# Optimization experiments

Hardware: AMD Instinct MI355X
Metric: run time of the kernel (lower is better)

## Reference

```python
import jax, jax.numpy as jnp
import numpy as np

D_MODEL = 1024
NUM_HEADS = 16
HEAD_DIM = D_MODEL // NUM_HEADS
B, T = 2, 2048


def setup_inputs() -> dict:
    key = jax.random.key(0)
    k1, k2, k3, k4, k5 = jax.random.split(key, 5)
    s = 1.0 / np.sqrt(D_MODEL)
    x = jax.random.normal(k1, (B, T, D_MODEL), dtype=jnp.float32)
    mask = jnp.ones((B, T), dtype=jnp.int32)
    W_qkv = jax.random.uniform(k2, (D_MODEL, 3 * D_MODEL), jnp.float32, -s, s)
    b_qkv = jax.random.uniform(k3, (3 * D_MODEL,), jnp.float32, -s, s)
    W_out = jax.random.uniform(k4, (D_MODEL, D_MODEL), jnp.float32, -s, s)
    b_out = jax.random.uniform(k5, (D_MODEL,), jnp.float32, -s, s)
    return {"x": x, "mask": mask, "W_qkv": W_qkv, "b_qkv": b_qkv,
            "W_out": W_out, "b_out": b_out}


def reference(x, mask, W_qkv, b_qkv, W_out, b_out):
    Bv, Tv, Dv = x.shape
    scale = HEAD_DIM ** -0.5
    qkv = x @ W_qkv + b_qkv                       # [B,T,3D]
    qkv = qkv.reshape(Bv, Tv, 3, NUM_HEADS, HEAD_DIM)
    qkv = jnp.transpose(qkv, (2, 0, 3, 1, 4))     # [3,B,H,T,hd]
    q, k, v = qkv[0], qkv[1], qkv[2]
    scores = jnp.einsum('bhqd,bhkd->bhqk', q, k) * scale  # [B,H,T,T]
    m = mask[:, None, None, :]                    # [B,1,1,T]
    scores = jnp.where(m == 0, -jnp.inf, scores)
    attn = jax.nn.softmax(scores, axis=-1)
    out = jnp.einsum('bhqk,bhkd->bhqd', attn, v)  # [B,H,T,hd]
    out = jnp.transpose(out, (0, 2, 1, 3)).reshape(Bv, Tv, Dv)
    return out @ W_out + b_out
```

## Files before the change

### kernel.cpp

```cpp
#include <hip/hip_runtime.h>

typedef __bf16 bf16;
typedef __bf16 bf16x8 __attribute__((ext_vector_type(8)));
typedef __bf16 bf16x4 __attribute__((ext_vector_type(4)));
typedef float  f32x4  __attribute__((ext_vector_type(4)));
typedef float  f32x16 __attribute__((ext_vector_type(16)));
typedef unsigned int u32x4 __attribute__((ext_vector_type(4)));

#define MFMA16(a, b, c) __builtin_amdgcn_mfma_f32_16x16x32_bf16((a), (b), (c), 0, 0, 0)
#define MFMA32(a, b, c) __builtin_amdgcn_mfma_f32_32x32x16_bf16((a), (b), (c), 0, 0, 0)

__device__ __forceinline__ float fexp2(float x) {
  return __builtin_amdgcn_exp2f(x);
}

__device__ __forceinline__ unsigned cvt_pk_bf16(float lo, float hi) {
  unsigned r;
  asm("v_cvt_pk_bf16_f32 %0, %1, %2" : "=v"(r) : "v"(lo), "v"(hi));
  return r;
}

__device__ __forceinline__ void gload_lds16(const bf16* g, bf16* l) {
  __builtin_amdgcn_global_load_lds(
      (const __attribute__((address_space(1))) void*)g,
      (__attribute__((address_space(3))) void*)l, 16, 0, 0);
}


__global__ __launch_bounds__(256) void cast_bf16_kernel(
    const float* __restrict__ in, bf16* __restrict__ out, int n4) {
  int i = blockIdx.x * 256 + threadIdx.x;
  if (i < n4) {
    float4 v = reinterpret_cast<const float4*>(in)[i];
    bf16x4 o;
    o[0] = (bf16)v.x; o[1] = (bf16)v.y; o[2] = (bf16)v.z; o[3] = (bf16)v.w;
    reinterpret_cast<bf16x4*>(out)[i] = o;
  }
}

__global__ __launch_bounds__(256) void transpose_cast_kernel(
    const float* __restrict__ W, bf16* __restrict__ Wt, int K, int N) {
  __shared__ bf16 tile[64 * 66];
  const int k0 = blockIdx.y * 64, n0 = blockIdx.x * 64;
  const int c = threadIdx.x & 63, rb = threadIdx.x >> 6;
#pragma unroll
  for (int p = 0; p < 16; ++p) {
    int r = p * 4 + rb;
    tile[c * 66 + r] = (bf16)W[(long)(k0 + r) * N + n0 + c];
  }
  __syncthreads();
#pragma unroll
  for (int p = 0; p < 16; ++p) {
    int r = p * 4 + rb;
    Wt[(long)(n0 + r) * K + k0 + c] = tile[r * 66 + c];
  }
}

template <int EPI>
__global__ __launch_bounds__(256, 2) void gemm_bt(
    const bf16* __restrict__ A, const bf16* __restrict__ Bt,
    const float* __restrict__ bias, bf16* __restrict__ oQ,
    bf16* __restrict__ oK, bf16* __restrict__ oVT, float* __restrict__ oC,
    int K) {
  __shared__ bf16 As[128 * 64];
  __shared__ bf16 Bs[128 * 64];
  const int tid = threadIdx.x, lane = tid & 63, wid = tid >> 6;
  const int wr = wid >> 1, wc = wid & 1;
  const int brow = blockIdx.x * 128, bcol = blockIdx.y * 128;
  const int srow = lane >> 3, scol8 = (lane & 7) * 8;
  const int c15 = lane & 15, g = lane >> 4;

  f32x4 acc[4][4];
#pragma unroll
  for (int m = 0; m < 4; ++m)
#pragma unroll
    for (int n = 0; n < 4; ++n) acc[m][n] = f32x4{0.f, 0.f, 0.f, 0.f};

  const bf16* Ab = A + (long)brow * K + scol8;
  const bf16* Bb = Bt + (long)bcol * K + scol8;

  for (int k0 = 0; k0 < K; k0 += 64) {
#pragma unroll
    for (int i = 0; i < 4; ++i) {
      int c = wid * 4 + i;
      int row = c * 8 + srow;
      gload_lds16(Ab + (long)row * K + k0, &As[c * 512]);
    }
#pragma unroll
    for (int i = 0; i < 4; ++i) {
      int c = wid * 4 + i;
      int row = c * 8 + srow;
      gload_lds16(Bb + (long)row * K + k0, &Bs[c * 512]);
    }
    __syncthreads();
#pragma unroll
    for (int kk = 0; kk < 64; kk += 32) {
      bf16x8 a[4], b[4];
#pragma unroll
      for (int m = 0; m < 4; ++m)
        a[m] = *(const bf16x8*)&As[(wr * 64 + m * 16 + c15) * 64 + kk + g * 8];
#pragma unroll
      for (int n = 0; n < 4; ++n)
        b[n] = *(const bf16x8*)&Bs[(wc * 64 + n * 16 + c15) * 64 + kk + g * 8];
#pragma unroll
      for (int m = 0; m < 4; ++m)
#pragma unroll
        for (int n = 0; n < 4; ++n)
          acc[m][n] = MFMA16(a[m], b[n], acc[m][n]);
    }
    __syncthreads();
  }

#pragma unroll
  for (int n = 0; n < 4; ++n) {
    const int col = bcol + wc * 64 + n * 16 + c15;
    const float bv = bias[col];
    if (EPI == 0) {
      const int which = col >> 10, wi = col & 1023, h = wi >> 6, d = wi & 63;
      const float sc = (which == 0) ? 0.18033688011112042f : 1.0f;
#pragma unroll
      for (int m = 0; m < 4; ++m) {
        const int row0 = brow + wr * 64 + m * 16 + g * 4;
        const int bb = row0 >> 11, t0 = row0 & 2047;
        const long hb = bb * 16 + h;
        if (which == 2) {
          bf16x4 pv;
#pragma unroll
          for (int r = 0; r < 4; ++r) pv[r] = (bf16)(acc[m][n][r] + bv);
          *(bf16x4*)&oVT[(hb * 64 + d) * 2048 + t0] = pv;
        } else {
          bf16* dst = ((which == 0) ? oQ : oK) + (hb * 2048 + t0) * 64 + d;
#pragma unroll
          for (int r = 0; r < 4; ++r)
            dst[(long)r * 64] = (bf16)((acc[m][n][r] + bv) * sc);
        }
      }
    } else {
#pragma unroll
      for (int m = 0; m < 4; ++m) {
        const long row = brow + wr * 64 + m * 16 + g * 4;
#pragma unroll
        for (int r = 0; r < 4; ++r) oC[(row + r) * 1024 + col] = acc[m][n][r] + bv;
      }
    }
  }
}

__global__ __launch_bounds__(256, 4) void attn_kernel(
    const bf16* __restrict__ Q, const bf16* __restrict__ K,
    const bf16* __restrict__ VT, const int* __restrict__ mask,
    float* __restrict__ O_part, float* __restrict__ ml_part) {
  __shared__ bf16 Kl[2][4096];
  __shared__ bf16 Vl[2][4096];
  __shared__ float sws[4][32];
  const int tid = threadIdx.x, lane = tid & 63, w = tid >> 6;
  const int col = lane & 31, hi = lane >> 5, c7 = col & 7;
  const int bid = blockIdx.x;
  const int swz = (bid & 7) * 128 + (bid >> 3);
  const int bh = swz >> 5, rem = swz & 31;
  const int s = rem & 1, qb = rem >> 1;
  const int b = bh >> 4, h = bh & 15;
  const int q0 = qb * 128 + w * 32;
  const int koff0 = s * 1024;

  const bf16* Kbase = K + (long)bh * 2048 * 64;
  const bf16* Vbase = VT + (long)bh * 64 * 2048;
  const int* mb = mask + b * 2048;

  const int srow = lane >> 3;
  const int xoff = ((lane & 7) ^ srow) << 3;

  auto stage = [&](int buf, int t) {
    const int koff = koff0 + t * 64;
#pragma unroll
    for (int i = 0; i < 2; ++i) {
      const int c = w * 2 + i;
      gload_lds16(Kbase + (long)(koff + c * 8 + srow) * 64 + xoff,
                  &Kl[buf][c * 512]);
      gload_lds16(Vbase + (long)(c * 8 + srow) * 2048 + koff + xoff,
                  &Vl[buf][c * 512]);
    }
  };

  const bf16* Qp = Q + ((long)bh * 2048 + q0 + col) * 64 + hi * 8;
  bf16x8 bq[4];
#pragma unroll
  for (int dc = 0; dc < 4; ++dc) bq[dc] = *(const bf16x8*)(Qp + dc * 16);

  f32x16 o0, o1;
#pragma unroll
  for (int r = 0; r < 16; ++r) { o0[r] = 0.f; o1[r] = 0.f; }
  float mrun = -1e30f, lrun = 0.f;

  stage(0, 0);
  for (int t = 0; t < 16; ++t) {
    const int cur = t & 1;
    __builtin_amdgcn_s_barrier();
    const int mvA = mb[koff0 + t * 64 + col];
    const int mvB = mb[koff0 + t * 64 + 32 + col];
    if (t < 15) {
      stage(cur ^ 1, t + 1);
      asm volatile("s_waitcnt vmcnt(6)" ::: "memory");
    } else {
      asm volatile("s_waitcnt vmcnt(0)" ::: "memory");
    }
    __builtin_amdgcn_s_barrier();

#pragma unroll
    for (int sub = 0; sub < 2; ++sub) {
      const int mv = (sub == 0) ? mvA : mvB;
      const bf16* Krow = &Kl[cur][(sub * 32 + col) * 64];
      bf16x8 ak0 = *(const bf16x8*)(Krow + (((0 + hi) ^ c7) << 3));
      bf16x8 ak1 = *(const bf16x8*)(Krow + (((2 + hi) ^ c7) << 3));
      bf16x8 ak2 = *(const bf16x8*)(Krow + (((4 + hi) ^ c7) << 3));
      bf16x8 ak3 = *(const bf16x8*)(Krow + (((6 + hi) ^ c7) << 3));
      f32x16 st;
#pragma unroll
      for (int r = 0; r < 16; ++r) st[r] = 0.f;
      __builtin_amdgcn_s_setprio(1);
      st = MFMA32(ak0, bq[0], st);
      st = MFMA32(ak1, bq[1], st);
      st = MFMA32(ak2, bq[2], st);
      st = MFMA32(ak3, bq[3], st);
      __builtin_amdgcn_s_setprio(0);
      unsigned km32 = (unsigned)__ballot(mv != 0);
      if (km32 != 0xffffffffu) {
        unsigned km = km32 >> (hi * 4);
#pragma unroll
        for (int r = 0; r < 16; ++r)
          if (!((km >> ((r & 3) + 8 * (r >> 2))) & 1)) st[r] = -1e30f;
      }
      float m01 = fmaxf(st[0], st[1]), m23 = fmaxf(st[2], st[3]);
      float m45 = fmaxf(st[4], st[5]), m67 = fmaxf(st[6], st[7]);
      float m89 = fmaxf(st[8], st[9]), mab = fmaxf(st[10], st[11]);
      float mcd = fmaxf(st[12], st[13]), mef = fmaxf(st[14], st[15]);
      float m0 = fmaxf(fmaxf(fmaxf(m01, m23), fmaxf(m45, m67)),
                       fmaxf(fmaxf(m89, mab), fmaxf(mcd, mef)));
      if (__any(m0 > mrun + 8.0f)) {
        float pm = fmaxf(m0, __shfl_xor(m0, 32));
        float mnew = fmaxf(mrun, pm);
        float scale = fexp2(mrun - mnew);
        mrun = mnew;
        lrun *= scale;
        if (hi == 0) sws[w][col] = scale;
        asm volatile("s_waitcnt lgkmcnt(0)" ::: "memory");
#pragma unroll
        for (int r = 0; r < 16; ++r) {
          float sc = sws[w][(r & 3) + 8 * (r >> 2) + 4 * hi];
          o0[r] *= sc; o1[r] *= sc;
        }
      }
#pragma unroll
      for (int r = 0; r < 16; ++r) st[r] = fexp2(st[r] - mrun);
      float s01 = st[0] + st[1], s23 = st[2] + st[3], s45 = st[4] + st[5];
      float s67 = st[6] + st[7], s89 = st[8] + st[9], sab = st[10] + st[11];
      float scd = st[12] + st[13], sef = st[14] + st[15];
      lrun += ((s01 + s23) + (s45 + s67)) + ((s89 + sab) + (scd + sef));
      unsigned d0 = cvt_pk_bf16(st[0], st[1]);
      unsigned d1 = cvt_pk_bf16(st[2], st[3]);
      unsigned d2 = cvt_pk_bf16(st[4], st[5]);
      unsigned d3 = cvt_pk_bf16(st[6], st[7]);
      unsigned d4 = cvt_pk_bf16(st[8], st[9]);
      unsigned d5 = cvt_pk_bf16(st[10], st[11]);
      unsigned d6 = cvt_pk_bf16(st[12], st[13]);
      unsigned d7 = cvt_pk_bf16(st[14], st[15]);
      unsigned g02 = (unsigned)__shfl_xor((int)(hi ? d0 : d2), 32);
      unsigned g13 = (unsigned)__shfl_xor((int)(hi ? d1 : d3), 32);
      unsigned g46 = (unsigned)__shfl_xor((int)(hi ? d4 : d6), 32);
      unsigned g57 = (unsigned)__shfl_xor((int)(hi ? d5 : d7), 32);
      u32x4 w0 = {hi ? g02 : d0, hi ? g13 : d1, hi ? d2 : g02, hi ? d3 : g13};
      u32x4 w1 = {hi ? g46 : d4, hi ? g57 : d5, hi ? d6 : g46, hi ? d7 : g57};
      bf16x8 pa0 = __builtin_bit_cast(bf16x8, w0);
      bf16x8 pa1 = __builtin_bit_cast(bf16x8, w1);
      const bf16* Vrow0 = &Vl[cur][col * 64];
      const bf16* Vrow1 = &Vl[cur][(col + 32) * 64];
      const int g0 = ((sub * 4 + hi) ^ c7) << 3;
      const int g1 = ((sub * 4 + 2 + hi) ^ c7) << 3;
      bf16x8 bv00 = *(const bf16x8*)(Vrow0 + g0);
      bf16x8 bv10 = *(const bf16x8*)(Vrow0 + g1);
      bf16x8 bv01 = *(const bf16x8*)(Vrow1 + g0);
      bf16x8 bv11 = *(const bf16x8*)(Vrow1 + g1);
      __builtin_amdgcn_s_setprio(1);
      o0 = MFMA32(pa0, bv00, o0);
      o0 = MFMA32(pa1, bv10, o0);
      o1 = MFMA32(pa0, bv01, o1);
      o1 = MFMA32(pa1, bv11, o1);
      __builtin_amdgcn_s_setprio(0);
    }
  }

  lrun += __shfl_xor(lrun, 32);
  if (hi == 0) {
    float2 v; v.x = mrun; v.y = lrun;
    *(float2*)&ml_part[((long)s * 65536 + bh * 2048 + q0 + col) * 2] = v;
  }
  float* Os = O_part + (long)s * 4194304;
#pragma unroll
  for (int r = 0; r < 16; ++r) {
    const int qr = (r & 3) + 8 * (r >> 2) + 4 * hi;
    long base = ((long)b * 2048 + q0 + qr) * 1024 + h * 64 + col;
    Os[base] = o0[r];
    Os[base + 32] = o1[r];
  }
}

__global__ __launch_bounds__(256) void attn_merge_kernel(
    const float* __restrict__ O_part, const float* __restrict__ ml_part,
    bf16* __restrict__ Aout) {
  const int i = blockIdx.x * 256 + threadIdx.x;
  const int qg = i >> 8;
  const int h = (i & 255) >> 4;
  const int bq = qg >> 11, t = qg & 2047;
  const int bh = bq * 16 + h;
  const float2 ml0 = *(const float2*)&ml_part[((long)bh * 2048 + t) * 2];
  const float2 ml1 = *(const float2*)&ml_part[((long)65536 + bh * 2048 + t) * 2];
  const float ms = fmaxf(ml0.x, ml1.x);
  const float w0 = fexp2(ml0.x - ms);
  const float w1 = fexp2(ml1.x - ms);
  const float inv = 1.0f / (w0 * ml0.y + w1 * ml1.y);
  float4 a = ((const float4*)O_part)[i];
  float4 c = ((const float4*)(O_part + 4194304))[i];
  bf16x4 o;
  o[0] = (bf16)((w0 * a.x + w1 * c.x) * inv);
  o[1] = (bf16)((w0 * a.y + w1 * c.y) * inv);
  o[2] = (bf16)((w0 * a.z + w1 * c.z) * inv);
  o[3] = (bf16)((w0 * a.w + w1 * c.w) * inv);
  ((bf16x4*)Aout)[i] = o;
}

extern "C" void kernel_launch(void* const* d_in, const int* in_sizes, int n_in,
                              void* d_out, int out_size, void* d_ws,
                              size_t ws_size, hipStream_t stream) {
  const float* x    = (const float*)d_in[0];
  const int*   mask = (const int*)d_in[1];
  const float* Wqkv = (const float*)d_in[2];
  const float* bqkv = (const float*)d_in[3];
  const float* Wout = (const float*)d_in[4];
  const float* bout = (const float*)d_in[5];
  float* out = (float*)d_out;

  char* ws = (char*)d_ws;
  bf16* xb    = (bf16*)(ws);
  bf16* wqkvT = (bf16*)(ws + (8u << 20));
  bf16* woutT = (bf16*)(ws + (14u << 20));
  bf16* Qb    = (bf16*)(ws + (16u << 20));
  bf16* Kb    = (bf16*)(ws + (24u << 20));
  bf16* VTb   = (bf16*)(ws + (32u << 20));
  float* Opart = (float*)(ws + (40u << 20));
  float* mlp   = (float*)(ws + (72u << 20));
  bf16* Aatt  = xb;

  cast_bf16_kernel<<<4096, 256, 0, stream>>>(x, xb, (4096 * 1024) / 4);
  transpose_cast_kernel<<<dim3(48, 16), 256, 0, stream>>>(Wqkv, wqkvT, 1024, 3072);
  transpose_cast_kernel<<<dim3(16, 16), 256, 0, stream>>>(Wout, woutT, 1024, 1024);
  gemm_bt<0><<<dim3(32, 24), 256, 0, stream>>>(xb, wqkvT, bqkv, Qb, Kb, VTb,
                                               nullptr, 1024);
  attn_kernel<<<1024, 256, 0, stream>>>(Qb, Kb, VTb, mask, Opart, mlp);
  attn_merge_kernel<<<4096, 256, 0, stream>>>(Opart, mlp, Aatt);
  gemm_bt<1><<<dim3(32, 8), 256, 0, stream>>>(Aatt, woutT, bout, nullptr,
                                              nullptr, nullptr, out, 1024);
}
```

Before: 138.0 us.

## Fuse split-K attention merge into attention kernel via LDS within 512-thread blocks

The two key-halves of each query block now run in one 512-thread workgroup, with waves 4-7 handling the second half. Partial outputs and the running max and sum are exchanged through LDS, and the first-half waves write the normalized bf16 result directly. This removes the separate merge kernel and the round trip of fp32 partial outputs through global memory. In exchange, LDS use per block doubles, blocks are larger so fewer may fit per CU, and half the waves sit idle during the merge.

```diff
diff --git a/kernel.cpp b/kernel.cpp
--- a/kernel.cpp
+++ b/kernel.cpp
@@ -146,21 +146,22 @@
   }
 }
 
-__global__ __launch_bounds__(256, 4) void attn_kernel(
+__global__ __launch_bounds__(512, 4) void attn_kernel(
     const bf16* __restrict__ Q, const bf16* __restrict__ K,
     const bf16* __restrict__ VT, const int* __restrict__ mask,
-    float* __restrict__ O_part, float* __restrict__ ml_part) {
-  __shared__ bf16 Kl[2][4096];
-  __shared__ bf16 Vl[2][4096];
-  __shared__ float sws[4][32];
+    bf16* __restrict__ Aout) {
+  __shared__ bf16 Kl[2][2][4096];
+  __shared__ bf16 Vl[2][2][4096];
+  __shared__ float sws[8][32];
+  __shared__ float mlL[2][4][2][32];
   const int tid = threadIdx.x, lane = tid & 63, w = tid >> 6;
+  const int wq = w & 3, s = w >> 2;
   const int col = lane & 31, hi = lane >> 5, c7 = col & 7;
   const int bid = blockIdx.x;
-  const int swz = (bid & 7) * 128 + (bid >> 3);
-  const int bh = swz >> 5, rem = swz & 31;
-  const int s = rem & 1, qb = rem >> 1;
+  const int swz = (bid & 7) * 64 + (bid >> 3);
+  const int bh = swz >> 4, qb = swz & 15;
   const int b = bh >> 4, h = bh & 15;
-  const int q0 = qb * 128 + w * 32;
+  const int q0 = qb * 128 + wq * 32;
   const int koff0 = s * 1024;
 
   const bf16* Kbase = K + (long)bh * 2048 * 64;
@@ -174,11 +175,11 @@
     const int koff = koff0 + t * 64;
 #pragma unroll
     for (int i = 0; i < 2; ++i) {
-      const int c = w * 2 + i;
+      const int c = wq * 2 + i;
       gload_lds16(Kbase + (long)(koff + c * 8 + srow) * 64 + xoff,
-                  &Kl[buf][c * 512]);
+                  &Kl[s][buf][c * 512]);
       gload_lds16(Vbase + (long)(c * 8 + srow) * 2048 + koff + xoff,
-                  &Vl[buf][c * 512]);
+                  &Vl[s][buf][c * 512]);
     }
   };
 
@@ -209,7 +210,7 @@
 #pragma unroll
     for (int sub = 0; sub < 2; ++sub) {
       const int mv = (sub == 0) ? mvA : mvB;
-      const bf16* Krow = &Kl[cur][(sub * 32 + col) * 64];
+      const bf16* Krow = &Kl[s][cur][(sub * 32 + col) * 64];
       bf16x8 ak0 = *(const bf16x8*)(Krow + (((0 + hi) ^ c7) << 3));
       bf16x8 ak1 = *(const bf16x8*)(Krow + (((2 + hi) ^ c7) << 3));
       bf16x8 ak2 = *(const bf16x8*)(Krow + (((4 + hi) ^ c7) << 3));
@@ -272,8 +273,8 @@
       u32x4 w1 = {hi ? g46 : d4, hi ? g57 : d5, hi ? d6 : g46, hi ? d7 : g57};
       bf16x8 pa0 = __builtin_bit_cast(bf16x8, w0);
       bf16x8 pa1 = __builtin_bit_cast(bf16x8, w1);
-      const bf16* Vrow0 = &Vl[cur][col * 64];
-      const bf16* Vrow1 = &Vl[cur][(col + 32) * 64];
+      const bf16* Vrow0 = &Vl[s][cur][col * 64];
+      const bf16* Vrow1 = &Vl[s][cur][(col + 32) * 64];
       const int g0 = ((sub * 4 + hi) ^ c7) << 3;
       const int g1 = ((sub * 4 + 2 + hi) ^ c7) << 3;
       bf16x8 bv00 = *(const bf16x8*)(Vrow0 + g0);
@@ -290,42 +291,35 @@
   }
 
   lrun += __shfl_xor(lrun, 32);
-  if (hi == 0) {
-    float2 v; v.x = mrun; v.y = lrun;
-    *(float2*)&ml_part[((long)s * 65536 + bh * 2048 + q0 + col) * 2] = v;
-  }
-  float* Os = O_part + (long)s * 4194304;
-#pragma unroll
-  for (int r = 0; r < 16; ++r) {
-    const int qr = (r & 3) + 8 * (r >> 2) + 4 * hi;
-    long base = ((long)b * 2048 + q0 + qr) * 1024 + h * 64 + col;
-    Os[base] = o0[r];
-    Os[base + 32] = o1[r];
-  }
-}
-
-__global__ __launch_bounds__(256) void attn_merge_kernel(
-    const float* __restrict__ O_part, const float* __restrict__ ml_part,
-    bf16* __restrict__ Aout) {
-  const int i = blockIdx.x * 256 + threadIdx.x;
-  const int qg = i >> 8;
-  const int h = (i & 255) >> 4;
-  const int bq = qg >> 11, t = qg & 2047;
-  const int bh = bq * 16 + h;
-  const float2 ml0 = *(const float2*)&ml_part[((long)bh * 2048 + t) * 2];
-  const float2 ml1 = *(const float2*)&ml_part[((long)65536 + bh * 2048 + t) * 2];
-  const float ms = fmaxf(ml0.x, ml1.x);
-  const float w0 = fexp2(ml0.x - ms);
-  const float w1 = fexp2(ml1.x - ms);
-  const float inv = 1.0f / (w0 * ml0.y + w1 * ml1.y);
-  float4 a = ((const float4*)O_part)[i];
-  float4 c = ((const float4*)(O_part + 4194304))[i];
-  bf16x4 o;
-  o[0] = (bf16)((w0 * a.x + w1 * c.x) * inv);
-  o[1] = (bf16)((w0 * a.y + w1 * c.y) * inv);
-  o[2] = (bf16)((w0 * a.z + w1 * c.z) * inv);
-  o[3] = (bf16)((w0 * a.w + w1 * c.w) * inv);
-  ((bf16x4*)Aout)[i] = o;
+  if (hi == 0) { mlL[s][wq][0][col] = mrun; mlL[s][wq][1][col] = lrun; }
+  __syncthreads();
+
+  float* Ol = (float*)Kl;
+  if (s == 1) {
+#pragma unroll
+    for (int r = 0; r < 16; ++r) {
+      Ol[(wq * 16 + r) * 128 + lane] = o0[r];
+      Ol[(wq * 16 + r) * 128 + 64 + lane] = o1[r];
+    }
+  }
+  __syncthreads();
+
+  if (s == 0) {
+#pragma unroll
+    for (int r = 0; r < 16; ++r) {
+      const int qr = (r & 3) + 8 * (r >> 2) + 4 * hi;
+      float m0v = mlL[0][wq][0][qr], l0v = mlL[0][wq][1][qr];
+      float m1v = mlL[1][wq][0][qr], l1v = mlL[1][wq][1][qr];
+      float ms = fmaxf(m0v, m1v);
+      float w0v = fexp2(m0v - ms), w1v = fexp2(m1v - ms);
+      float inv = 1.0f / (w0v * l0v + w1v * l1v);
+      float v0 = (w0v * o0[r] + w1v * Ol[(wq * 16 + r) * 128 + lane]) * inv;
+      float v1 = (w0v * o1[r] + w1v * Ol[(wq * 16 + r) * 128 + 64 + lane]) * inv;
+      long base = ((long)b * 2048 + q0 + qr) * 1024 + h * 64 + col;
+      Aout[base] = (bf16)v0;
+      Aout[base + 32] = (bf16)v1;
+    }
+  }
 }
 
 extern "C" void kernel_launch(void* const* d_in, const int* in_sizes, int n_in,
@@ -346,8 +340,6 @@
   bf16* Qb    = (bf16*)(ws + (16u << 20));
   bf16* Kb    = (bf16*)(ws + (24u << 20));
   bf16* VTb   = (bf16*)(ws + (32u << 20));
-  float* Opart = (float*)(ws + (40u << 20));
-  float* mlp   = (float*)(ws + (72u << 20));
   bf16* Aatt  = xb;
 
   cast_bf16_kernel<<<4096, 256, 0, stream>>>(x, xb, (4096 * 1024) / 4);
@@ -355,8 +347,7 @@
   transpose_cast_kernel<<<dim3(16, 16), 256, 0, stream>>>(Wout, woutT, 1024, 1024);
   gemm_bt<0><<<dim3(32, 24), 256, 0, stream>>>(xb, wqkvT, bqkv, Qb, Kb, VTb,
                                                nullptr, 1024);
-  attn_kernel<<<1024, 256, 0, stream>>>(Qb, Kb, VTb, mask, Opart, mlp);
-  attn_merge_kernel<<<4096, 256, 0, stream>>>(Opart, mlp, Aatt);
+  attn_kernel<<<512, 512, 0, stream>>>(Qb, Kb, VTb, mask, Aatt);
   gemm_bt<1><<<dim3(32, 8), 256, 0, stream>>>(Aatt, woutT, bout, nullptr,
                                               nullptr, nullptr, out, 1024);
 }
```

After: 133.1 us. -3.5%, faster.
